# Performance work log

Measured on AMD Instinct MI355X. Metric: run time of the kernel, lower is better.

The kernel has to match this reference:

```python
import jax, jax.numpy as jnp
import numpy as np

NEG_INF = -jnp.inf


def setup_inputs() -> dict:
    key = jax.random.key(0)
    k1, k2, k3 = jax.random.split(key, 3)
    B, S, D_IN, E = 16, 2048, 1024, 1024
    feats = jax.random.normal(k1, (B * S, D_IN), dtype=jnp.float32)
    masks = (jax.random.uniform(k2, (B * S, 1)) > 0.1).astype(jnp.float32)
    W = jax.random.normal(k3, (D_IN, E), dtype=jnp.float32) * 0.02
    b = jnp.zeros((E,), dtype=jnp.float32)
    return {"feats": feats, "masks": masks, "W": W, "b": b, "num_steps": S}


def reference(feats, masks, W, b, num_steps):
    B = feats.shape[0] // num_steps
    feats = feats.reshape(B, num_steps, feats.shape[-1])          # (B,S,D_in)
    x = jnp.einsum("bsd,de->bse", feats, W) + b                   # feats_proj

    masks_seq = (masks.reshape(B, num_steps, -1) != 0).any(-1)    # (B,S) bool
    masks_f = masks_seq.astype(x.dtype)

    # position ids: cumsum of mask, zeroed where mask == 0
    position_ids = jnp.where(masks_seq, jnp.cumsum(masks_f, axis=1), 0.0)

    # episodic attention mask: episode_start[j] = last k<=j with mask==0 (default 0)
    idx = jnp.arange(num_steps)                                   # (S,)
    start_cand = jnp.where(masks_seq, 0, idx[None, :])            # (B,S)
    ep_start = jax.lax.associative_scan(jnp.maximum, start_cand, axis=1)  # cummax
    allowed = (idx[None, None, :] >= ep_start[:, :, None]) & (
        idx[None, None, :] <= idx[None, :, None]
    )                                                             # (B,S,S)
    attn_mask = jnp.where(allowed, 0.0, NEG_INF).astype(x.dtype)
    return x, position_ids, attn_mask
```

## Files before the change

### kernel.cpp

```cpp
#include <hip/hip_runtime.h>


typedef unsigned int uint;
typedef unsigned short ushort;
typedef __attribute__((ext_vector_type(8))) short bf16x8;
typedef __attribute__((ext_vector_type(4))) float f32x4;
typedef __attribute__((ext_vector_type(8))) ushort u16x8;

__device__ __forceinline__ ushort f2bf_rtn(float x) {
    uint u = __float_as_uint(x);
    uint r = (u + 0x7FFFu + ((u >> 16) & 1u)) >> 16;
    return (ushort)r;
}

__device__ __forceinline__ int lidx(int row, int chunk) {
    return row * 64 + ((chunk ^ (row & 7)) << 3);
}

#define LDS_BARRIER() do {                                        \
    __builtin_amdgcn_sched_barrier(0);                            \
    asm volatile("s_waitcnt lgkmcnt(0)" ::: "memory");            \
    __builtin_amdgcn_s_barrier();                                 \
    __builtin_amdgcn_sched_barrier(0);                            \
} while (0)

__global__ __launch_bounds__(256) void wsplit1_k(
    const float* __restrict__ W, ushort* __restrict__ Wh, int K, int N)
{
    __shared__ float tile[32][33];
    const int n0 = blockIdx.x * 32, k0 = blockIdx.y * 32;
    const int t = threadIdx.x;
    {
        const int nn = t & 31, kk = t >> 5;
        #pragma unroll
        for (int i = 0; i < 4; ++i)
            tile[kk + i * 8][nn] = W[(size_t)(k0 + kk + i * 8) * N + n0 + nn];
    }
    __syncthreads();
    {
        const int kk = t & 31, nn = t >> 5;
        #pragma unroll
        for (int i = 0; i < 4; ++i) {
            float x = tile[kk][nn + i * 8];
            Wh[(size_t)(n0 + nn + i * 8) * K + k0 + kk] = f2bf_rtn(x);
        }
    }
}

__global__ __launch_bounds__(256) void scan_k(
    const float* __restrict__ masks, float* __restrict__ pos_out,
    int* __restrict__ ep_out, int S)
{
    const int b = blockIdx.x, t = threadIdx.x;
    const float* mrow = masks + (size_t)b * S;

    float ls[8]; int lm[8]; bool on8[8];
    float csum = 0.0f; int cmax = 0;
    #pragma unroll
    for (int e = 0; e < 8; ++e) {
        const int j = t * 8 + e;
        const bool on = (mrow[j] != 0.0f);
        on8[e] = on;
        csum += on ? 1.0f : 0.0f;
        if (!on && j > cmax) cmax = j;
        ls[e] = csum;
        lm[e] = cmax;
    }
    __shared__ float ps[256];
    __shared__ int   pm[256];
    ps[t] = csum; pm[t] = cmax;
    __syncthreads();
    for (int off = 1; off < 256; off <<= 1) {
        float s = 0.0f; int m = 0;
        if (t >= off) { s = ps[t - off]; m = pm[t - off]; }
        __syncthreads();
        if (t >= off) { ps[t] += s; pm[t] = (m > pm[t]) ? m : pm[t]; }
        __syncthreads();
    }
    const float esum = (t == 0) ? 0.0f : ps[t - 1];
    const int   emax = (t == 0) ? 0    : pm[t - 1];
    #pragma unroll
    for (int e = 0; e < 8; ++e) {
        const int j = t * 8 + e;
        pos_out[(size_t)b * S + j] = on8[e] ? (esum + ls[e]) : 0.0f;
        const int ep = (lm[e] > emax) ? lm[e] : emax;
        ep_out[(size_t)b * S + j] = ep;
    }
}

__global__ __launch_bounds__(256, 1) void mfma_gemm20_k(
    const float* __restrict__ A, const ushort* __restrict__ Bh,
    const float* __restrict__ bias, float* __restrict__ C,
    const int* __restrict__ ep_ws, float* __restrict__ mask_out,
    int M, int N, int K, int S)
{
    __shared__ ushort Ls[2][128 * 64];

    const int tid  = threadIdx.x;
    const int lane = tid & 63, wv = tid >> 6;
    const int wr   = wv >> 1,  wc = wv & 1;

    const int lin = blockIdx.x;
    const int xcd = lin & 7, sblk = lin >> 3;
    const int bm  = xcd * 32 + (sblk >> 3);
    const int bn  = sblk & 7;

    const int kc   = tid & 3;
    const int q0   = tid >> 2;
    const int row0 = ((q0 & 3) << 2) | ((q0 >> 2) & 3) | (q0 & ~15);
    const int row1 = row0 | 64;

    const float*  Ag  = A  + (size_t)(bm * 128) * K;
    const ushort* Bhg = Bh + (size_t)(bn * 128) * K;

    float4 a_lo[2], a_hi[2];
    u16x8  b_st[2];

    auto gload = [&](int kt) {
        const int kb = kt * 32 + kc * 8;
        const float* p0 = Ag + (size_t)row0 * K + kb;
        const float* p1 = Ag + (size_t)row1 * K + kb;
        a_lo[0] = *(const float4*)p0;       a_hi[0] = *(const float4*)(p0 + 4);
        a_lo[1] = *(const float4*)p1;       a_hi[1] = *(const float4*)(p1 + 4);
        b_st[0] = *(const u16x8*)(Bhg + (size_t)row0 * K + kb);
        b_st[1] = *(const u16x8*)(Bhg + (size_t)row1 * K + kb);
    };

    auto lwrite = [&](int buf) {
        #pragma unroll
        for (int i = 0; i < 2; ++i) {
            const int row = i ? row1 : row0;
            float xs[8] = {a_lo[i].x, a_lo[i].y, a_lo[i].z, a_lo[i].w,
                           a_hi[i].x, a_hi[i].y, a_hi[i].z, a_hi[i].w};
            u16x8 vh;
            #pragma unroll
            for (int j = 0; j < 8; ++j)
                vh[j] = f2bf_rtn(xs[j]);
            *(u16x8*)&Ls[buf][lidx(row, kc)]     = vh;
            *(u16x8*)&Ls[buf][lidx(row, 4 + kc)] = b_st[i];
        }
    };

    f32x4 acc[4][4] = {};

    const int arow0 = wr * 64 + (lane & 15);
    const int brow0 = wc * 64 + (lane & 15);
    const int fq    = lane >> 4;

    const int mrow  = lin * 16 + (tid >> 4);
    const int irow  = mrow & (S - 1);
    const int ep    = ep_ws[mrow];
    const int l16   = tid & 15;
    f32x4* mbase    = (f32x4*)(mask_out + (size_t)mrow * S) + l16;
    const float NEG_BIG = -1.0e30f;

    gload(0);
    lwrite(0);
    __syncthreads();

    int cur = 0;
    const int NT = K / 32;
    for (int kt = 0; kt < NT; ++kt) {
        if (kt + 1 < NT) gload(kt + 1);

        {
            const int f  = l16 + 16 * kt;
            const int c0 = f * 4;
            f32x4 v;
            if (c0 >= ep && c0 + 3 <= irow) {
                v = (f32x4){0.0f, 0.0f, 0.0f, 0.0f};
            } else if (c0 + 3 < ep || c0 > irow) {
                v = (f32x4){NEG_BIG, NEG_BIG, NEG_BIG, NEG_BIG};
            } else {
                v[0] = (c0     >= ep && c0     <= irow) ? 0.0f : NEG_BIG;
                v[1] = (c0 + 1 >= ep && c0 + 1 <= irow) ? 0.0f : NEG_BIG;
                v[2] = (c0 + 2 >= ep && c0 + 2 <= irow) ? 0.0f : NEG_BIG;
                v[3] = (c0 + 3 >= ep && c0 + 3 <= irow) ? 0.0f : NEG_BIG;
            }
            __builtin_nontemporal_store(v, mbase + 16 * kt);
        }

        bf16x8 fb[4], ah[4];
        #pragma unroll
        for (int ni = 0; ni < 4; ++ni)
            fb[ni] = *(const bf16x8*)&Ls[cur][lidx(brow0 + ni * 16, 4 + fq)];
        #pragma unroll
        for (int mi = 0; mi < 4; ++mi)
            ah[mi] = *(const bf16x8*)&Ls[cur][lidx(arow0 + mi * 16, fq)];
        #pragma unroll
        for (int mi = 0; mi < 4; ++mi)
            #pragma unroll
            for (int ni = 0; ni < 4; ++ni)
                acc[mi][ni] = __builtin_amdgcn_mfma_f32_16x16x32_bf16(
                    ah[mi], fb[ni], acc[mi][ni], 0, 0, 0);

        if (kt + 1 < NT) {
            lwrite(cur ^ 1);
            LDS_BARRIER();
            cur ^= 1;
        }
    }

    const int crow = (lane >> 4) * 4;
    #pragma unroll
    for (int ni = 0; ni < 4; ++ni) {
        const int n = bn * 128 + wc * 64 + ni * 16 + (lane & 15);
        const float bv = bias[n];
        #pragma unroll
        for (int mi = 0; mi < 4; ++mi) {
            const int m0 = bm * 128 + wr * 64 + mi * 16 + crow;
            #pragma unroll
            for (int jj = 0; jj < 4; ++jj)
                __builtin_nontemporal_store(acc[mi][ni][jj] + bv,
                                            &C[(size_t)(m0 + jj) * N + n]);
        }
    }
}

#define BM 128
#define BN 128
#define BK 16

__global__ __launch_bounds__(256) void proj_gemm_k(
    const float* __restrict__ A, const float* __restrict__ B,
    const float* __restrict__ bias, float* __restrict__ C,
    int M, int N, int K)
{
    constexpr int LA = BM + 4;
    constexpr int LB = BN + 4;
    __shared__ __align__(16) float As[2][BK][LA];
    __shared__ __align__(16) float Bs[2][BK][LB];

    const int tid = threadIdx.x;
    const int bn  = blockIdx.x;
    const int bm  = blockIdx.y;
    const int ty  = tid >> 4;
    const int tx  = tid & 15;

    const float* Ag = A + (size_t)bm * BM * K;
    const float* Bg = B + (size_t)bn * BN;

    const int fa_r = tid >> 2;
    const int fa_c = (tid & 3) * 4;
    const int fb_k = tid >> 5;
    const int fb_c = (tid & 31) * 4;

    const int NT = K / BK;
    float acc[2][2][4][4] = {};
    float4 a0r, a1r, b0r, b1r;

    auto write_tile = [&](int buf) {
        As[buf][fa_c + 0][fa_r] = a0r.x;
        As[buf][fa_c + 1][fa_r] = a0r.y;
        As[buf][fa_c + 2][fa_r] = a0r.z;
        As[buf][fa_c + 3][fa_r] = a0r.w;
        As[buf][fa_c + 0][fa_r + 64] = a1r.x;
        As[buf][fa_c + 1][fa_r + 64] = a1r.y;
        As[buf][fa_c + 2][fa_r + 64] = a1r.z;
        As[buf][fa_c + 3][fa_r + 64] = a1r.w;
        *(float4*)&Bs[buf][fb_k][fb_c]     = b0r;
        *(float4*)&Bs[buf][fb_k + 8][fb_c] = b1r;
    };
    auto load_tile = [&](int kt) {
        const float* ap = Ag + kt * BK;
        a0r = *(const float4*)(ap + (size_t)fa_r * K + fa_c);
        a1r = *(const float4*)(ap + (size_t)(fa_r + 64) * K + fa_c);
        const float* bp = Bg + (size_t)kt * BK * N;
        b0r = *(const float4*)(bp + (size_t)fb_k * N + fb_c);
        b1r = *(const float4*)(bp + (size_t)(fb_k + 8) * N + fb_c);
    };

    load_tile(0);
    write_tile(0);
    __syncthreads();

    int cur = 0;
    for (int kt = 0; kt < NT; ++kt) {
        if (kt + 1 < NT) load_tile(kt + 1);
        #pragma unroll
        for (int k = 0; k < BK; ++k) {
            float4 x0 = *(const float4*)&As[cur][k][ty * 4];
            float4 x1 = *(const float4*)&As[cur][k][64 + ty * 4];
            float4 y0 = *(const float4*)&Bs[cur][k][tx * 4];
            float4 y1 = *(const float4*)&Bs[cur][k][64 + tx * 4];
            float avv[2][4] = {{x0.x, x0.y, x0.z, x0.w}, {x1.x, x1.y, x1.z, x1.w}};
            float bvv[2][4] = {{y0.x, y0.y, y0.z, y0.w}, {y1.x, y1.y, y1.z, y1.w}};
            #pragma unroll
            for (int mi = 0; mi < 2; ++mi)
                #pragma unroll
                for (int i = 0; i < 4; ++i)
                    #pragma unroll
                    for (int ni = 0; ni < 2; ++ni)
                        #pragma unroll
                        for (int jj = 0; jj < 4; ++jj)
                            acc[mi][ni][i][jj] = fmaf(avv[mi][i], bvv[ni][jj], acc[mi][ni][i][jj]);
        }
        if (kt + 1 < NT) {
            write_tile(cur ^ 1);
            __syncthreads();
            cur ^= 1;
        }
    }

    #pragma unroll
    for (int ni = 0; ni < 2; ++ni) {
        const int n = bn * BN + ni * 64 + tx * 4;
        float4 bv = *(const float4*)&bias[n];
        #pragma unroll
        for (int mi = 0; mi < 2; ++mi) {
            #pragma unroll
            for (int i = 0; i < 4; ++i) {
                const int m = bm * BM + mi * 64 + ty * 4 + i;
                float4 o;
                o.x = acc[mi][ni][i][0] + bv.x;
                o.y = acc[mi][ni][i][1] + bv.y;
                o.z = acc[mi][ni][i][2] + bv.z;
                o.w = acc[mi][ni][i][3] + bv.w;
                *(float4*)(C + (size_t)m * N + n) = o;
            }
        }
    }
}

__global__ __launch_bounds__(256) void episodic_mask_k(
    const float* __restrict__ masks, float* __restrict__ pos_out,
    float* __restrict__ mask_out, int S)
{
    const int i = blockIdx.x;
    const int b = blockIdx.y;
    const int t = threadIdx.x;
    const float* mrow = masks + (size_t)b * S;

    float sum = 0.0f;
    int   mx  = 0;
    for (int j = t; j <= i; j += 256) {
        const bool on = (mrow[j] != 0.0f);
        sum += on ? 1.0f : 0.0f;
        if (!on && j > mx) mx = j;
    }
    #pragma unroll
    for (int off = 32; off > 0; off >>= 1) {
        sum += __shfl_down(sum, off, 64);
        int o = __shfl_down(mx, off, 64);
        mx = (o > mx) ? o : mx;
    }
    __shared__ float wsum[4];
    __shared__ int   wmax[4];
    __shared__ int   s_ep;
    const int wid = t >> 6, lane = t & 63;
    if (lane == 0) { wsum[wid] = sum; wmax[wid] = mx; }
    __syncthreads();
    if (t == 0) {
        float ts = wsum[0] + wsum[1] + wsum[2] + wsum[3];
        int tm = wmax[0];
        tm = (wmax[1] > tm) ? wmax[1] : tm;
        tm = (wmax[2] > tm) ? wmax[2] : tm;
        tm = (wmax[3] > tm) ? wmax[3] : tm;
        s_ep = tm;
        pos_out[(size_t)b * S + i] = (mrow[i] != 0.0f) ? ts : 0.0f;
    }
    __syncthreads();
    const int ep = s_ep;
    const float NEG_BIG = -1.0e30f;
    float4* orow = (float4*)(mask_out + ((size_t)b * S + i) * S);
    const int nf = S >> 2;
    for (int f = t; f < nf; f += 256) {
        const int j0 = f * 4;
        float4 v;
        v.x = (j0     >= ep && j0     <= i) ? 0.0f : NEG_BIG;
        v.y = (j0 + 1 >= ep && j0 + 1 <= i) ? 0.0f : NEG_BIG;
        v.z = (j0 + 2 >= ep && j0 + 2 <= i) ? 0.0f : NEG_BIG;
        v.w = (j0 + 3 >= ep && j0 + 3 <= i) ? 0.0f : NEG_BIG;
        orow[f] = v;
    }
}

extern "C" void kernel_launch(void* const* d_in, const int* in_sizes, int n_in,
                              void* d_out, int out_size, void* d_ws, size_t ws_size,
                              hipStream_t stream)
{
    const float* feats = (const float*)d_in[0];
    const float* masks = (const float*)d_in[1];
    const float* W     = (const float*)d_in[2];
    const float* bias  = (const float*)d_in[3];

    const int M = in_sizes[1];
    const int K = in_sizes[0] / M;
    const int N = in_sizes[3];
    const int S = out_size / M - N - 1;
    const int B = M / S;

    float* x_out    = (float*)d_out;
    float* pos_out  = x_out + (size_t)M * N;
    float* mask_out = pos_out + M;

    const size_t w_w   = (size_t)K * N * sizeof(ushort);
    const size_t w_all = w_w + (size_t)M * sizeof(int);

    if (ws_size >= w_all && S == 2048 && (M % 16) == 0 && (K % 32) == 0) {
        ushort* Wh = (ushort*)d_ws;
        int*    ep = (int*)(Wh + (size_t)K * N);
        wsplit1_k<<<dim3(N / 32, K / 32), 256, 0, stream>>>(W, Wh, K, N);
        scan_k<<<B, 256, 0, stream>>>(masks, pos_out, ep, S);
        const int nblk = (M / 128) * (N / 128);
        mfma_gemm20_k<<<nblk, 256, 0, stream>>>(
            feats, Wh, bias, x_out, ep, mask_out, M, N, K, S);
    } else {
        proj_gemm_k<<<dim3(N / BN, M / BM), 256, 0, stream>>>(feats, W, bias, x_out, M, N, K);
        episodic_mask_k<<<dim3(S, B), 256, 0, stream>>>(masks, pos_out, mask_out, S);
    }
}
```

Before: 148.9 us.

## Prefetch fp32 A tiles two k-steps ahead with double register sets

The GEMM main loop is unrolled by two and uses two register sets for the fp32 A operand, so A loads are issued two k-iterations ahead of their LDS write while B stays one iteration ahead. This aims to hide the global-memory latency of the large fp32 activation stream behind more MFMA work. It raises register pressure (an extra 16 floats per thread) and now requires K to be a multiple of 64 for the fast path.

```diff
diff --git a/kernel.cpp b/kernel.cpp
--- a/kernel.cpp
+++ b/kernel.cpp
@@ -88,7 +88,7 @@
     }
 }
 
-__global__ __launch_bounds__(256, 1) void mfma_gemm20_k(
+__global__ __launch_bounds__(256, 1) void mfma_gemm21_k(
     const float* __restrict__ A, const ushort* __restrict__ Bh,
     const float* __restrict__ bias, float* __restrict__ C,
     const int* __restrict__ ep_ws, float* __restrict__ mask_out,
@@ -113,25 +113,49 @@
     const float*  Ag  = A  + (size_t)(bm * 128) * K;
     const ushort* Bhg = Bh + (size_t)(bn * 128) * K;
 
-    float4 a_lo[2], a_hi[2];
+    float4 aL0[2], aH0[2], aL1[2], aH1[2];
     u16x8  b_st[2];
 
-    auto gload = [&](int kt) {
+    auto gloadA0 = [&](int kt) {
         const int kb = kt * 32 + kc * 8;
         const float* p0 = Ag + (size_t)row0 * K + kb;
         const float* p1 = Ag + (size_t)row1 * K + kb;
-        a_lo[0] = *(const float4*)p0;       a_hi[0] = *(const float4*)(p0 + 4);
-        a_lo[1] = *(const float4*)p1;       a_hi[1] = *(const float4*)(p1 + 4);
+        aL0[0] = *(const float4*)p0;  aH0[0] = *(const float4*)(p0 + 4);
+        aL0[1] = *(const float4*)p1;  aH0[1] = *(const float4*)(p1 + 4);
+    };
+    auto gloadA1 = [&](int kt) {
+        const int kb = kt * 32 + kc * 8;
+        const float* p0 = Ag + (size_t)row0 * K + kb;
+        const float* p1 = Ag + (size_t)row1 * K + kb;
+        aL1[0] = *(const float4*)p0;  aH1[0] = *(const float4*)(p0 + 4);
+        aL1[1] = *(const float4*)p1;  aH1[1] = *(const float4*)(p1 + 4);
+    };
+    auto gloadB = [&](int kt) {
+        const int kb = kt * 32 + kc * 8;
         b_st[0] = *(const u16x8*)(Bhg + (size_t)row0 * K + kb);
         b_st[1] = *(const u16x8*)(Bhg + (size_t)row1 * K + kb);
     };
 
-    auto lwrite = [&](int buf) {
+    auto lwrite0 = [&](int buf) {
         #pragma unroll
         for (int i = 0; i < 2; ++i) {
             const int row = i ? row1 : row0;
-            float xs[8] = {a_lo[i].x, a_lo[i].y, a_lo[i].z, a_lo[i].w,
-                           a_hi[i].x, a_hi[i].y, a_hi[i].z, a_hi[i].w};
+            float xs[8] = {aL0[i].x, aL0[i].y, aL0[i].z, aL0[i].w,
+                           aH0[i].x, aH0[i].y, aH0[i].z, aH0[i].w};
+            u16x8 vh;
+            #pragma unroll
+            for (int j = 0; j < 8; ++j)
+                vh[j] = f2bf_rtn(xs[j]);
+            *(u16x8*)&Ls[buf][lidx(row, kc)]     = vh;
+            *(u16x8*)&Ls[buf][lidx(row, 4 + kc)] = b_st[i];
+        }
+    };
+    auto lwrite1 = [&](int buf) {
+        #pragma unroll
+        for (int i = 0; i < 2; ++i) {
+            const int row = i ? row1 : row0;
+            float xs[8] = {aL1[i].x, aL1[i].y, aL1[i].z, aL1[i].w,
+                           aH1[i].x, aH1[i].y, aH1[i].z, aH1[i].w};
             u16x8 vh;
             #pragma unroll
             for (int j = 0; j < 8; ++j)
@@ -154,32 +178,24 @@
     f32x4* mbase    = (f32x4*)(mask_out + (size_t)mrow * S) + l16;
     const float NEG_BIG = -1.0e30f;
 
-    gload(0);
-    lwrite(0);
-    __syncthreads();
-
-    int cur = 0;
-    const int NT = K / 32;
-    for (int kt = 0; kt < NT; ++kt) {
-        if (kt + 1 < NT) gload(kt + 1);
-
-        {
-            const int f  = l16 + 16 * kt;
-            const int c0 = f * 4;
-            f32x4 v;
-            if (c0 >= ep && c0 + 3 <= irow) {
-                v = (f32x4){0.0f, 0.0f, 0.0f, 0.0f};
-            } else if (c0 + 3 < ep || c0 > irow) {
-                v = (f32x4){NEG_BIG, NEG_BIG, NEG_BIG, NEG_BIG};
-            } else {
-                v[0] = (c0     >= ep && c0     <= irow) ? 0.0f : NEG_BIG;
-                v[1] = (c0 + 1 >= ep && c0 + 1 <= irow) ? 0.0f : NEG_BIG;
-                v[2] = (c0 + 2 >= ep && c0 + 2 <= irow) ? 0.0f : NEG_BIG;
-                v[3] = (c0 + 3 >= ep && c0 + 3 <= irow) ? 0.0f : NEG_BIG;
-            }
-            __builtin_nontemporal_store(v, mbase + 16 * kt);
-        }
-
+    auto mask_store = [&](int kt) {
+        const int f  = l16 + 16 * kt;
+        const int c0 = f * 4;
+        f32x4 v;
+        if (c0 >= ep && c0 + 3 <= irow) {
+            v = (f32x4){0.0f, 0.0f, 0.0f, 0.0f};
+        } else if (c0 + 3 < ep || c0 > irow) {
+            v = (f32x4){NEG_BIG, NEG_BIG, NEG_BIG, NEG_BIG};
+        } else {
+            v[0] = (c0     >= ep && c0     <= irow) ? 0.0f : NEG_BIG;
+            v[1] = (c0 + 1 >= ep && c0 + 1 <= irow) ? 0.0f : NEG_BIG;
+            v[2] = (c0 + 2 >= ep && c0 + 2 <= irow) ? 0.0f : NEG_BIG;
+            v[3] = (c0 + 3 >= ep && c0 + 3 <= irow) ? 0.0f : NEG_BIG;
+        }
+        __builtin_nontemporal_store(v, mbase + 16 * kt);
+    };
+
+    auto compute = [&](int cur) {
         bf16x8 fb[4], ah[4];
         #pragma unroll
         for (int ni = 0; ni < 4; ++ni)
@@ -193,11 +209,36 @@
             for (int ni = 0; ni < 4; ++ni)
                 acc[mi][ni] = __builtin_amdgcn_mfma_f32_16x16x32_bf16(
                     ah[mi], fb[ni], acc[mi][ni], 0, 0, 0);
-
+    };
+
+    gloadA0(0);
+    gloadB(0);
+    lwrite0(0);
+    gloadA1(1);
+    __syncthreads();
+
+    const int NT = K / 32;
+    int cur = 0;
+    for (int kt = 0; kt < NT; kt += 2) {
+        if (kt + 1 < NT) gloadB(kt + 1);
+        mask_store(kt);
+        compute(cur);
         if (kt + 1 < NT) {
-            lwrite(cur ^ 1);
+            lwrite1(cur ^ 1);
+            if (kt + 2 < NT) gloadA0(kt + 2);
             LDS_BARRIER();
             cur ^= 1;
+        }
+        if (kt + 1 < NT) {
+            if (kt + 2 < NT) gloadB(kt + 2);
+            mask_store(kt + 1);
+            compute(cur);
+            if (kt + 2 < NT) {
+                lwrite0(cur ^ 1);
+                if (kt + 3 < NT) gloadA1(kt + 3);
+                LDS_BARRIER();
+                cur ^= 1;
+            }
         }
     }
 
@@ -397,13 +438,13 @@
     const size_t w_w   = (size_t)K * N * sizeof(ushort);
     const size_t w_all = w_w + (size_t)M * sizeof(int);
 
-    if (ws_size >= w_all && S == 2048 && (M % 16) == 0 && (K % 32) == 0) {
+    if (ws_size >= w_all && S == 2048 && (M % 16) == 0 && (K % 64) == 0) {
         ushort* Wh = (ushort*)d_ws;
         int*    ep = (int*)(Wh + (size_t)K * N);
         wsplit1_k<<<dim3(N / 32, K / 32), 256, 0, stream>>>(W, Wh, K, N);
         scan_k<<<B, 256, 0, stream>>>(masks, pos_out, ep, S);
         const int nblk = (M / 128) * (N / 128);
-        mfma_gemm20_k<<<nblk, 256, 0, stream>>>(
+        mfma_gemm21_k<<<nblk, 256, 0, stream>>>(
             feats, Wh, bias, x_out, ep, mask_out, M, N, K, S);
     } else {
         proj_gemm_k<<<dim3(N / BN, M / BM), 256, 0, stream>>>(feats, W, bias, x_out, M, N, K);
```

After: 156.5 us. +5.1%, slower.
